# Kernel tuning notes

Measured on AMD Instinct MI355X. Metric: run time of the kernel, lower is better.

Reference implementation:

```python
import jax, jax.numpy as jnp
import numpy as np
from jax import lax

K = 33  # avgpool kernel
P = 16  # padding
EPS = 1e-08


def _box_sum(x):
    # Sum over 33x33 windows, stride 1, zero padding 16 on H and W (NCHW).
    return lax.reduce_window(
        x, 0.0, lax.add,
        window_dimensions=(1, 1, K, K),
        window_strides=(1, 1, 1, 1),
        padding=((0, 0), (0, 0), (P, P), (P, P)),
    )


def setup_inputs() -> dict:
    key = jax.random.key(0)
    input_tensor = jax.random.normal(key, (64, 1, 80, 3000), dtype=jnp.float32)
    return {"input_tensor": input_tensor}


def reference(input_tensor):
    B, C, H, W = input_tensor.shape
    # count_include_pad=False: divide by number of VALID elements per window.
    counts = _box_sum(jnp.ones((1, 1, H, W), dtype=input_tensor.dtype))
    local_mean = _box_sum(input_tensor) / counts
    centered = input_tensor - local_mean
    local_var = _box_sum(centered * centered) / counts
    local_std = jnp.sqrt(local_var)
    return centered / (local_std + EPS)
```

## Files before the change

### kernel.cpp

```cpp
#include <hip/hip_runtime.h>
#include <hip/hip_bf16.h>
#include <math.h>

#define BB 64
#define HH 80
#define WW 3000
#define RAD 16
#define TW 96
#define XSW 68
#define HXS 116
#define NSTRIP 32
#define NT 1024
#define EPSF 1e-8f

#define XS_WORDS (HH * XSW)
#define HXP_OFF  XS_WORDS
#define HXP_WORDS (TW * HXS)
#define ICH_OFF  (XS_WORDS + HXP_WORDS)
#define TOT_WORDS (ICH_OFF + HH)

typedef float f32x2 __attribute__((ext_vector_type(2)));
typedef float f32x4 __attribute__((ext_vector_type(4)));

__device__ __forceinline__ float bflo(uint32_t w) { return __uint_as_float(w << 16); }
__device__ __forceinline__ float bfhi(uint32_t w) { return __uint_as_float(w & 0xffff0000u); }
__device__ __forceinline__ uint32_t packbf2(float lo, float hi) {
    union { __hip_bfloat162 h2; uint32_t u; } u;
    u.h2 = __hip_bfloat162(__float2bfloat16(lo), __float2bfloat16(hi));
    return u.u;
}
__device__ __forceinline__ f32x2 uw(uint32_t w) {
    f32x2 r; r.x = bflo(w); r.y = bfhi(w); return r;
}

#define E4(V, J) ((J) == 0 ? (V).x : ((J) == 1 ? (V).y : ((J) == 2 ? (V).z : (V).w)))
#define W20(Q) E4((Q) < 4 ? v0 : (Q) < 8 ? v1 : (Q) < 12 ? v2 : (Q) < 16 ? v3 : v4, (Q) & 3)
#define W48(Q) E4((Q) < 4 ? R0 : (Q) < 8 ? R1 : (Q) < 12 ? R2 : (Q) < 16 ? R3 : (Q) < 20 ? R4 : \
                  (Q) < 24 ? R5 : (Q) < 28 ? R6 : (Q) < 32 ? R7 : (Q) < 36 ? R8 : \
                  (Q) < 40 ? R9 : (Q) < 44 ? R10 : R11, (Q) & 3)

__global__ __launch_bounds__(NT, 8)
void localnorm_kernel(const float* __restrict__ in, float* __restrict__ out) {
    extern __shared__ uint32_t smem[];
    uint32_t* Hxp = smem + HXP_OFF;
    float* inv_ch = (float*)(smem + ICH_OFF);

    const int t     = threadIdx.x;
    const int strip = blockIdx.x % NSTRIP;
    const int b     = blockIdx.x / NSTRIP;
    const int c0    = strip * TW;
    const float* inb = in + (size_t)b * (HH * WW);

    if (t < HH) {
        int lo = max(t - RAD, 0), hi = min(t + RAD, HH - 1);
        inv_ch[t] = 1.0f / (float)(hi - lo + 1);
    }
    if (t < 768) {
        const int col = t >> 3;
        const int c8  = t & 7;
        const int off = col * HXS + ((c8 < 4) ? (c8 * 4) : (96 + (c8 - 4) * 4));
        *(uint4*)(Hxp + off) = make_uint4(0u, 0u, 0u, 0u);
    }

    const int w    = t >> 6;
    const int lane = t & 63;

    {
        #pragma unroll
        for (int i = 0; i < 3; ++i) {
            const int task = i * 64 + lane;
            if (i < 2 || task < 160) {
                const int row = 5 * w + (task >> 5);
                const int q   = task & 31;
                const int gc  = c0 - 16 + 4 * q;
                uint2 w2;
                if (gc >= 0 && gc + 4 <= WW) {
                    float4 v = *(const float4*)(inb + (size_t)row * WW + gc);
                    w2.x = packbf2(v.x, v.y);
                    w2.y = packbf2(v.z, v.w);
                } else {
                    float p0 = (gc     >= 0 && gc     < WW) ? inb[(size_t)row * WW + gc]     : 0.f;
                    float p1 = (gc + 1 >= 0 && gc + 1 < WW) ? inb[(size_t)row * WW + gc + 1] : 0.f;
                    float p2 = (gc + 2 >= 0 && gc + 2 < WW) ? inb[(size_t)row * WW + gc + 2] : 0.f;
                    float p3 = (gc + 3 >= 0 && gc + 3 < WW) ? inb[(size_t)row * WW + gc + 3] : 0.f;
                    w2.x = packbf2(p0, p1);
                    w2.y = packbf2(p2, p3);
                }
                *(uint2*)(smem + row * XSW + 2 * q) = w2;
            }
        }
    }

    if (lane < 60) {
        const int row = 5 * w + lane / 12;
        const int seg = lane % 12;
        const uint32_t* xr = smem + row * XSW + seg * 4;
        uint4 v0 = *(const uint4*)(xr);
        uint4 v1 = *(const uint4*)(xr + 4);
        uint4 v2 = *(const uint4*)(xr + 8);
        uint4 v3 = *(const uint4*)(xr + 12);
        uint4 v4 = *(const uint4*)(xr + 16);
        float l16 = bflo(W20(16));
        f32x2 pA; pA.x = l16;       pA.y = 0.f;
        f32x2 qA; qA.x = l16 * l16; qA.y = 0.f;
        f32x2 pB; pB.x = 0.f; pB.y = 0.f;
        f32x2 qB; qB.x = 0.f; qB.y = 0.f;
        #pragma unroll
        for (int q = 0; q < 16; q += 2) {
            f32x2 uA = uw(W20(q));
            f32x2 uB = uw(W20(q + 1));
            pA += uA;      pB += uB;
            qA += uA * uA; qB += uB * uB;
        }
        f32x2 ps = pA + pB, qs = qA + qB;
        float ax  = ps.x + ps.y;
        float axx = qs.x + qs.y;
        uint32_t* hw = Hxp + (seg * 8) * HXS + row + 16;
        #pragma unroll
        for (int k = 0; k < 4; ++k) {
            uint32_t wS = W20(k), wE = W20(k + 16);
            float lS = bflo(wS), hE = bfhi(wE);
            float a1x  = ax - lS + hE;
            float a1xx = axx - lS * lS + hE * hE;
            hw[(2 * k) * HXS]     = packbf2(ax, axx);
            hw[(2 * k + 1) * HXS] = packbf2(a1x, a1xx);
            if (k != 3) {
                float hS = bfhi(wS), lN = bflo(W20(k + 17));
                ax  = a1x - hS + lN;
                axx = a1xx - hS * hS + lN * lN;
            }
        }
    }
    __syncthreads();

    {
        const int c    = t % TW;
        const int band = t / TW;
        const int gc   = c0 + c;
        if (band < 5 && gc < WW) {
            const int r0 = band * 16;
            const uint32_t* hp = Hxp + c * HXS + r0;
            uint4 R0  = *(const uint4*)(hp);
            uint4 R1  = *(const uint4*)(hp + 4);
            uint4 R2  = *(const uint4*)(hp + 8);
            uint4 R3  = *(const uint4*)(hp + 12);
            uint4 R4  = *(const uint4*)(hp + 16);
            uint4 R5  = *(const uint4*)(hp + 20);
            uint4 R6  = *(const uint4*)(hp + 24);
            uint4 R7  = *(const uint4*)(hp + 28);
            uint4 R8  = *(const uint4*)(hp + 32);
            uint4 R9  = *(const uint4*)(hp + 36);
            uint4 R10 = *(const uint4*)(hp + 40);
            uint4 R11 = *(const uint4*)(hp + 44);
            f32x2 aA = uw(W48(32));
            f32x2 aB; aB.x = 0.f; aB.y = 0.f;
            #pragma unroll
            for (int q = 0; q < 32; q += 2) {
                aA += uw(W48(q));
                aB += uw(W48(q + 1));
            }
            f32x2 acc = aA + aB;
            const float icw = 1.0f / (float)(min(gc + RAD, WW - 1) - max(gc - RAD, 0) + 1);
            const int  xwoff  = (c + 16) >> 1;
            const bool hiHf   = ((c + 16) & 1) != 0;
            float* outb = out + (size_t)b * (HH * WW);
            #pragma unroll
            for (int k = 0; k < 16; ++k) {
                const int r = r0 + k;
                const float ninv = inv_ch[r] * icw;
                f32x2 me = acc * ninv;
                float var = fmaxf(me.y - me.x * me.x, 1e-24f);
#if defined(__has_builtin) && __has_builtin(__builtin_amdgcn_rsqf)
                float isd = __builtin_amdgcn_rsqf(var);
#else
                float isd = __builtin_amdgcn_rcpf(__builtin_amdgcn_sqrtf(var) + EPSF);
#endif
                uint32_t xw = smem[r * XSW + xwoff];
                float xv = hiHf ? bfhi(xw) : bflo(xw);
                outb[(size_t)r * WW + gc] = (xv - me.x) * isd;
                if (k != 15) {
                    acc += uw(W48(k + 33)) - uw(W48(k));
                }
            }
        }
    }
}

extern "C" void kernel_launch(void* const* d_in, const int* in_sizes, int n_in,
                              void* d_out, int out_size, void* d_ws, size_t ws_size,
                              hipStream_t stream) {
    const float* in = (const float*)d_in[0];
    float* out = (float*)d_out;

    const size_t lds_bytes = (size_t)TOT_WORDS * sizeof(uint32_t);
    static bool attr_set = false;
    if (!attr_set) {
        (void)hipFuncSetAttribute((const void*)localnorm_kernel,
                                  hipFuncAttributeMaxDynamicSharedMemorySize,
                                  (int)lds_bytes);
        attr_set = true;
    }

    dim3 grid(BB * NSTRIP);
    dim3 block(NT);
    localnorm_kernel<<<grid, block, lds_bytes, stream>>>(in, out);
}
```

Before: 39.53 us.

## Process four strips per block with prefetch of next strip and lightweight barriers

Each block now loops over four consecutive column strips instead of one, cutting the grid from 2048 to 512 blocks and reusing the zero-initialised LDS and per-row constants. During the horizontal pass it issues dummy global loads to warm the cache lines of the next strip. Full __syncthreads are replaced with a custom barrier that waits only on LDS counters, and the load and horizontal-sum thread mappings are reorganised. The cost is serialised per-block work and fewer blocks to fill the GPU, and the dummy loads are never consumed, so they add extra memory traffic.

```diff
diff --git a/kernel.cpp b/kernel.cpp
--- a/kernel.cpp
+++ b/kernel.cpp
@@ -9,7 +9,8 @@
 #define TW 96
 #define XSW 68
 #define HXS 116
-#define NSTRIP 32
+#define S_PER_BLK 4
+#define NKGRP 8
 #define NT 1024
 #define EPSF 1e-8f
 
@@ -20,7 +21,6 @@
 #define TOT_WORDS (ICH_OFF + HH)
 
 typedef float f32x2 __attribute__((ext_vector_type(2)));
-typedef float f32x4 __attribute__((ext_vector_type(4)));
 
 __device__ __forceinline__ float bflo(uint32_t w) { return __uint_as_float(w << 16); }
 __device__ __forceinline__ float bfhi(uint32_t w) { return __uint_as_float(w & 0xffff0000u); }
@@ -33,6 +33,13 @@
     f32x2 r; r.x = bflo(w); r.y = bfhi(w); return r;
 }
 
+__device__ __forceinline__ void softbar() {
+    __builtin_amdgcn_sched_barrier(0);
+    asm volatile("s_waitcnt lgkmcnt(0)" ::: "memory");
+    __builtin_amdgcn_s_barrier();
+    __builtin_amdgcn_sched_barrier(0);
+}
+
 #define E4(V, J) ((J) == 0 ? (V).x : ((J) == 1 ? (V).y : ((J) == 2 ? (V).z : (V).w)))
 #define W20(Q) E4((Q) < 4 ? v0 : (Q) < 8 ? v1 : (Q) < 12 ? v2 : (Q) < 16 ? v3 : v4, (Q) & 3)
 #define W48(Q) E4((Q) < 4 ? R0 : (Q) < 8 ? R1 : (Q) < 12 ? R2 : (Q) < 16 ? R3 : (Q) < 20 ? R4 : \
@@ -45,10 +52,10 @@
     uint32_t* Hxp = smem + HXP_OFF;
     float* inv_ch = (float*)(smem + ICH_OFF);
 
-    const int t     = threadIdx.x;
-    const int strip = blockIdx.x % NSTRIP;
-    const int b     = blockIdx.x / NSTRIP;
-    const int c0    = strip * TW;
+    const int t      = threadIdx.x;
+    const int kgrp   = blockIdx.x & (NKGRP - 1);
+    const int b      = blockIdx.x / NKGRP;
+    const int strip0 = kgrp * S_PER_BLK;
     const float* inb = in + (size_t)b * (HH * WW);
 
     if (t < HH) {
@@ -62,127 +69,144 @@
         *(uint4*)(Hxp + off) = make_uint4(0u, 0u, 0u, 0u);
     }
 
-    const int w    = t >> 6;
-    const int lane = t & 63;
-
-    {
-        #pragma unroll
-        for (int i = 0; i < 3; ++i) {
-            const int task = i * 64 + lane;
-            if (i < 2 || task < 160) {
-                const int row = 5 * w + (task >> 5);
-                const int q   = task & 31;
-                const int gc  = c0 - 16 + 4 * q;
-                uint2 w2;
-                if (gc >= 0 && gc + 4 <= WW) {
-                    float4 v = *(const float4*)(inb + (size_t)row * WW + gc);
-                    w2.x = packbf2(v.x, v.y);
-                    w2.y = packbf2(v.z, v.w);
-                } else {
-                    float p0 = (gc     >= 0 && gc     < WW) ? inb[(size_t)row * WW + gc]     : 0.f;
-                    float p1 = (gc + 1 >= 0 && gc + 1 < WW) ? inb[(size_t)row * WW + gc + 1] : 0.f;
-                    float p2 = (gc + 2 >= 0 && gc + 2 < WW) ? inb[(size_t)row * WW + gc + 2] : 0.f;
-                    float p3 = (gc + 3 >= 0 && gc + 3 < WW) ? inb[(size_t)row * WW + gc + 3] : 0.f;
-                    w2.x = packbf2(p0, p1);
-                    w2.y = packbf2(p2, p3);
-                }
-                *(uint2*)(smem + row * XSW + 2 * q) = w2;
+    #pragma unroll 1
+    for (int s = 0; s < S_PER_BLK; ++s) {
+        const int c0 = (strip0 + s) * TW;
+
+        {
+            #pragma unroll
+            for (int it = 0; it < 3; ++it) {
+                const int id = t + it * NT;
+                if (it < 2 || id < 2560) {
+                    const int row = id >> 5;
+                    const int q   = id & 31;
+                    const int gc  = c0 - 16 + 4 * q;
+                    uint2 w2;
+                    if (gc >= 0 && gc + 4 <= WW) {
+                        float4 v = *(const float4*)(inb + (size_t)row * WW + gc);
+                        w2.x = packbf2(v.x, v.y);
+                        w2.y = packbf2(v.z, v.w);
+                    } else {
+                        float p0 = (gc     >= 0 && gc     < WW) ? inb[(size_t)row * WW + gc]     : 0.f;
+                        float p1 = (gc + 1 >= 0 && gc + 1 < WW) ? inb[(size_t)row * WW + gc + 1] : 0.f;
+                        float p2 = (gc + 2 >= 0 && gc + 2 < WW) ? inb[(size_t)row * WW + gc + 2] : 0.f;
+                        float p3 = (gc + 3 >= 0 && gc + 3 < WW) ? inb[(size_t)row * WW + gc + 3] : 0.f;
+                        w2.x = packbf2(p0, p1);
+                        w2.y = packbf2(p2, p3);
+                    }
+                    *(uint2*)(smem + row * XSW + 2 * q) = w2;
+                }
             }
         }
-    }
-
-    if (lane < 60) {
-        const int row = 5 * w + lane / 12;
-        const int seg = lane % 12;
-        const uint32_t* xr = smem + row * XSW + seg * 4;
-        uint4 v0 = *(const uint4*)(xr);
-        uint4 v1 = *(const uint4*)(xr + 4);
-        uint4 v2 = *(const uint4*)(xr + 8);
-        uint4 v3 = *(const uint4*)(xr + 12);
-        uint4 v4 = *(const uint4*)(xr + 16);
-        float l16 = bflo(W20(16));
-        f32x2 pA; pA.x = l16;       pA.y = 0.f;
-        f32x2 qA; qA.x = l16 * l16; qA.y = 0.f;
-        f32x2 pB; pB.x = 0.f; pB.y = 0.f;
-        f32x2 qB; qB.x = 0.f; qB.y = 0.f;
-        #pragma unroll
-        for (int q = 0; q < 16; q += 2) {
-            f32x2 uA = uw(W20(q));
-            f32x2 uB = uw(W20(q + 1));
-            pA += uA;      pB += uB;
-            qA += uA * uA; qB += uB * uB;
-        }
-        f32x2 ps = pA + pB, qs = qA + qB;
-        float ax  = ps.x + ps.y;
-        float axx = qs.x + qs.y;
-        uint32_t* hw = Hxp + (seg * 8) * HXS + row + 16;
-        #pragma unroll
-        for (int k = 0; k < 4; ++k) {
-            uint32_t wS = W20(k), wE = W20(k + 16);
-            float lS = bflo(wS), hE = bfhi(wE);
-            float a1x  = ax - lS + hE;
-            float a1xx = axx - lS * lS + hE * hE;
-            hw[(2 * k) * HXS]     = packbf2(ax, axx);
-            hw[(2 * k + 1) * HXS] = packbf2(a1x, a1xx);
-            if (k != 3) {
-                float hS = bfhi(wS), lN = bflo(W20(k + 17));
-                ax  = a1x - hS + lN;
-                axx = a1xx - hS * hS + lN * lN;
+        softbar();
+
+        if (s + 1 < S_PER_BLK && t < 400) {
+            const int row = t / 5;
+            const int j   = t - row * 5;
+            const int cg  = (strip0 + s + 1) * TW - 16 + ((j < 4) ? j * 32 : 127);
+            const int col = min(cg, WW - 1);
+            const float* ap = inb + (size_t)row * WW + col;
+            float dummy;
+            asm volatile("global_load_dword %0, %1, off"
+                         : "=v"(dummy) : "v"((uint64_t)(uintptr_t)ap) : "memory");
+        }
+
+        {
+            const int row = t % HH;
+            const int seg = t / HH;
+            if (seg < 12) {
+                const uint32_t* xr = smem + row * XSW + seg * 4;
+                uint4 v0 = *(const uint4*)(xr);
+                uint4 v1 = *(const uint4*)(xr + 4);
+                uint4 v2 = *(const uint4*)(xr + 8);
+                uint4 v3 = *(const uint4*)(xr + 12);
+                uint4 v4 = *(const uint4*)(xr + 16);
+                float l16 = bflo(W20(16));
+                f32x2 pA; pA.x = l16;       pA.y = 0.f;
+                f32x2 qA; qA.x = l16 * l16; qA.y = 0.f;
+                f32x2 pB; pB.x = 0.f; pB.y = 0.f;
+                f32x2 qB; qB.x = 0.f; qB.y = 0.f;
+                #pragma unroll
+                for (int q = 0; q < 16; q += 2) {
+                    f32x2 uA = uw(W20(q));
+                    f32x2 uB = uw(W20(q + 1));
+                    pA += uA;      pB += uB;
+                    qA += uA * uA; qB += uB * uB;
+                }
+                f32x2 ps = pA + pB, qs = qA + qB;
+                float ax  = ps.x + ps.y;
+                float axx = qs.x + qs.y;
+                uint32_t* hw = Hxp + (seg * 8) * HXS + row + 16;
+                #pragma unroll
+                for (int k = 0; k < 4; ++k) {
+                    uint32_t wS = W20(k), wE = W20(k + 16);
+                    float lS = bflo(wS), hE = bfhi(wE);
+                    float a1x  = ax - lS + hE;
+                    float a1xx = axx - lS * lS + hE * hE;
+                    hw[(2 * k) * HXS]     = packbf2(ax, axx);
+                    hw[(2 * k + 1) * HXS] = packbf2(a1x, a1xx);
+                    if (k != 3) {
+                        float hS = bfhi(wS), lN = bflo(W20(k + 17));
+                        ax  = a1x - hS + lN;
+                        axx = a1xx - hS * hS + lN * lN;
+                    }
+                }
             }
         }
-    }
-    __syncthreads();
-
-    {
-        const int c    = t % TW;
-        const int band = t / TW;
-        const int gc   = c0 + c;
-        if (band < 5 && gc < WW) {
-            const int r0 = band * 16;
-            const uint32_t* hp = Hxp + c * HXS + r0;
-            uint4 R0  = *(const uint4*)(hp);
-            uint4 R1  = *(const uint4*)(hp + 4);
-            uint4 R2  = *(const uint4*)(hp + 8);
-            uint4 R3  = *(const uint4*)(hp + 12);
-            uint4 R4  = *(const uint4*)(hp + 16);
-            uint4 R5  = *(const uint4*)(hp + 20);
-            uint4 R6  = *(const uint4*)(hp + 24);
-            uint4 R7  = *(const uint4*)(hp + 28);
-            uint4 R8  = *(const uint4*)(hp + 32);
-            uint4 R9  = *(const uint4*)(hp + 36);
-            uint4 R10 = *(const uint4*)(hp + 40);
-            uint4 R11 = *(const uint4*)(hp + 44);
-            f32x2 aA = uw(W48(32));
-            f32x2 aB; aB.x = 0.f; aB.y = 0.f;
-            #pragma unroll
-            for (int q = 0; q < 32; q += 2) {
-                aA += uw(W48(q));
-                aB += uw(W48(q + 1));
+        softbar();
+
+        {
+            const int c    = t % TW;
+            const int band = t / TW;
+            const int gc   = c0 + c;
+            if (band < 5 && gc < WW) {
+                const int r0 = band * 16;
+                const uint32_t* hp = Hxp + c * HXS + r0;
+                uint4 R0  = *(const uint4*)(hp);
+                uint4 R1  = *(const uint4*)(hp + 4);
+                uint4 R2  = *(const uint4*)(hp + 8);
+                uint4 R3  = *(const uint4*)(hp + 12);
+                uint4 R4  = *(const uint4*)(hp + 16);
+                uint4 R5  = *(const uint4*)(hp + 20);
+                uint4 R6  = *(const uint4*)(hp + 24);
+                uint4 R7  = *(const uint4*)(hp + 28);
+                uint4 R8  = *(const uint4*)(hp + 32);
+                uint4 R9  = *(const uint4*)(hp + 36);
+                uint4 R10 = *(const uint4*)(hp + 40);
+                uint4 R11 = *(const uint4*)(hp + 44);
+                f32x2 aA = uw(W48(32));
+                f32x2 aB; aB.x = 0.f; aB.y = 0.f;
+                #pragma unroll
+                for (int q = 0; q < 32; q += 2) {
+                    aA += uw(W48(q));
+                    aB += uw(W48(q + 1));
+                }
+                f32x2 acc = aA + aB;
+                const float icw = 1.0f / (float)(min(gc + RAD, WW - 1) - max(gc - RAD, 0) + 1);
+                const int  xwoff  = (c + 16) >> 1;
+                const bool hiHf   = ((c + 16) & 1) != 0;
+                float* outb = out + (size_t)b * (HH * WW);
+                #pragma unroll
+                for (int k = 0; k < 16; ++k) {
+                    const int r = r0 + k;
+                    const float ninv = inv_ch[r] * icw;
+                    f32x2 me = acc * ninv;
+                    float var = fmaxf(me.y - me.x * me.x, 1e-24f);
+#if defined(__has_builtin) && __has_builtin(__builtin_amdgcn_rsqf)
+                    float isd = __builtin_amdgcn_rsqf(var);
+#else
+                    float isd = __builtin_amdgcn_rcpf(__builtin_amdgcn_sqrtf(var) + EPSF);
+#endif
+                    uint32_t xw = smem[r * XSW + xwoff];
+                    float xv = hiHf ? bfhi(xw) : bflo(xw);
+                    outb[(size_t)r * WW + gc] = (xv - me.x) * isd;
+                    if (k != 15) {
+                        acc += uw(W48(k + 33)) - uw(W48(k));
+                    }
+                }
             }
-            f32x2 acc = aA + aB;
-            const float icw = 1.0f / (float)(min(gc + RAD, WW - 1) - max(gc - RAD, 0) + 1);
-            const int  xwoff  = (c + 16) >> 1;
-            const bool hiHf   = ((c + 16) & 1) != 0;
-            float* outb = out + (size_t)b * (HH * WW);
-            #pragma unroll
-            for (int k = 0; k < 16; ++k) {
-                const int r = r0 + k;
-                const float ninv = inv_ch[r] * icw;
-                f32x2 me = acc * ninv;
-                float var = fmaxf(me.y - me.x * me.x, 1e-24f);
-#if defined(__has_builtin) && __has_builtin(__builtin_amdgcn_rsqf)
-                float isd = __builtin_amdgcn_rsqf(var);
-#else
-                float isd = __builtin_amdgcn_rcpf(__builtin_amdgcn_sqrtf(var) + EPSF);
-#endif
-                uint32_t xw = smem[r * XSW + xwoff];
-                float xv = hiHf ? bfhi(xw) : bflo(xw);
-                outb[(size_t)r * WW + gc] = (xv - me.x) * isd;
-                if (k != 15) {
-                    acc += uw(W48(k + 33)) - uw(W48(k));
-                }
-            }
-        }
+        }
+        if (s + 1 < S_PER_BLK) softbar();
     }
 }
 
@@ -201,7 +225,7 @@
         attr_set = true;
     }
 
-    dim3 grid(BB * NSTRIP);
+    dim3 grid(BB * NKGRP);
     dim3 block(NT);
     localnorm_kernel<<<grid, block, lds_bytes, stream>>>(in, out);
 }
```

Measured after the change: 96.03 us. 2.43x slower.
